# Optimization experiments

Hardware: AMD Instinct MI355X
Metric: run time of the kernel (lower is better)

The kernel has to match this reference:

```python
import jax, jax.numpy as jnp
import numpy as np

B_SZ, L, D_MODEL, D_STATE = 8, 2048, 1024, 64
LN_EPS = 1e-5


def setup_inputs() -> dict:
    key = jax.random.key(0)
    ks = jax.random.split(key, 12)
    x = jax.random.normal(ks[0], (B_SZ, L, D_MODEL), dtype=jnp.float32)
    # input projection (nn.Linear)
    W_in = jax.random.normal(ks[1], (D_MODEL, D_MODEL), dtype=jnp.float32) / np.sqrt(D_MODEL)
    b_in = jnp.zeros((D_MODEL,), dtype=jnp.float32)
    # LayerNorm affine
    gamma = jnp.ones((D_MODEL,), dtype=jnp.float32)
    beta = jnp.zeros((D_MODEL,), dtype=jnp.float32)
    # SSM params as real/imag pairs (torch stores cfloat); init per _init_state_space
    A_re = -jax.random.uniform(ks[2], (D_STATE,), dtype=jnp.float32) * 0.1
    A_im = jax.random.normal(ks[3], (D_STATE,), dtype=jnp.float32) * 0.1
    B_re = jax.random.normal(ks[4], (D_STATE,), dtype=jnp.float32) * 0.0004
    B_im = jax.random.normal(ks[5], (D_STATE,), dtype=jnp.float32) * 0.0004
    C_re = jax.random.normal(ks[6], (D_MODEL, D_STATE), dtype=jnp.float32) * 0.0004
    C_im = jax.random.normal(ks[7], (D_MODEL, D_STATE), dtype=jnp.float32) * 0.0004
    D_re = jax.random.normal(ks[8], (D_MODEL,), dtype=jnp.float32) * 0.02
    D_im = jax.random.normal(ks[9], (D_MODEL,), dtype=jnp.float32) * 0.02
    return {"x": x, "W_in": W_in, "b_in": b_in, "gamma": gamma, "beta": beta,
            "A_re": A_re, "A_im": A_im, "B_re": B_re, "B_im": B_im,
            "C_re": C_re, "C_im": C_im, "D_re": D_re, "D_im": D_im}


def _forward(x, W_in, b_in, gamma, beta, A_re, A_im, B_re, B_im, C_re, C_im, D_re, D_im):
    # input projection + LayerNorm
    x = jnp.einsum('bld,de->ble', x, W_in.T) + b_in
    mu = jnp.mean(x, axis=-1, keepdims=True)
    var = jnp.mean(jnp.square(x - mu), axis=-1, keepdims=True)
    x = (x - mu) * jax.lax.rsqrt(var + LN_EPS) * gamma + beta

    Lc = x.shape[1]
    A = A_re + 1j * A_im          # (N,)
    Bp = B_re + 1j * B_im         # (N,)
    Cp = C_re + 1j * C_im         # (M, N)
    Dp = D_re + 1j * D_im         # (M,)
    # A^l via exp(l * log A) -> (L, N), stable for autodiff
    pows = jnp.exp(jnp.arange(Lc, dtype=jnp.float32)[:, None] * jnp.log(A)[None, :])
    # fused kernel generation: K[l, m] = sum_n A^l[n] * B[n] * C[m, n]  (+ D broadcast on all taps, per source)
    K = jnp.einsum('ln,n,mn->lm', pows, Bp, Cp) + Dp[None, :]  # (L, M) complex

    # causal depthwise long convolution via FFT: y[t, m] = sum_{s<=t} K[s, m] * x[t-s, m]
    n = 2 * Lc
    Xf = jnp.fft.fft(x.astype(jnp.complex64), n=n, axis=1)   # (B, 2L, M)
    Kf = jnp.fft.fft(K, n=n, axis=0)                          # (2L, M)
    y = jnp.fft.ifft(Xf * Kf[None], axis=1)[:, :Lc, :].real   # real part (standard S4 convention)

    return y.astype(x.dtype) + x  # dropout=0 (eval); residual


def reference(x, W_in, b_in, gamma, beta, A_re, A_im, B_re, B_im, C_re, C_im, D_re, D_im):
    return _forward(x, W_in, b_in, gamma, beta, A_re, A_im, B_re, B_im, C_re, C_im, D_re, D_im)
```

## Files before the change

kernel.cpp:

```cpp
#include <hip/hip_runtime.h>
#include <stdint.h>


typedef __attribute__((ext_vector_type(8))) short short8;
typedef __attribute__((ext_vector_type(8))) unsigned short ushort8;
typedef __attribute__((ext_vector_type(4))) float f32x4;
typedef unsigned short ushort;

#define L_SEQ 2048
#define DM    1024
#define TT    8
#define NC    16
#define CL    128

__device__ __forceinline__ ushort f2bf(float f) {
  uint32_t u = __builtin_bit_cast(uint32_t, f);
  u += 0x7FFFu + ((u >> 16) & 1u);
  return (ushort)(u >> 16);
}
__device__ __forceinline__ float bf2f(ushort u) {
  uint32_t w = ((uint32_t)u) << 16;
  return __builtin_bit_cast(float, w);
}
__device__ __forceinline__ void gload16(const void* g, void* lds_p) {
  __builtin_amdgcn_global_load_lds(
      (const __attribute__((address_space(1))) uint32_t*)g,
      (__attribute__((address_space(3))) uint32_t*)lds_p, 16, 0, 0);
}

__global__ __launch_bounds__(256) void cvt_and_kgen(
    const float* __restrict__ x, const float* __restrict__ W,
    ushort* __restrict__ Xbf, ushort* __restrict__ Wbf,
    const float* __restrict__ A_re, const float* __restrict__ A_im,
    const float* __restrict__ B_re, const float* __restrict__ B_im,
    const float* __restrict__ C_re, const float* __restrict__ C_im,
    float* __restrict__ Khat, int nx8, int nw8, int cvtBlocks) {
  int blk = blockIdx.x;
  int tid = threadIdx.x;
  if (blk < cvtBlocks) {
    int i = blk * 256 + tid;
    const float* src; ushort* dst; int idx;
    if (i < nx8) { src = x; dst = Xbf; idx = i; }
    else         { src = W; dst = Wbf; idx = i - nx8; if (idx >= nw8) return; }
    const f32x4* s = (const f32x4*)src + (size_t)idx * 2;
    f32x4 a = s[0], b = s[1];
    ushort8 o;
    #pragma unroll
    for (int e = 0; e < 4; ++e) { o[e] = f2bf(a[e]); o[4 + e] = f2bf(b[e]); }
    *(ushort8*)(dst + (size_t)idx * 8) = o;
    return;
  }
  int s = blk - cvtBlocks;
  __shared__ float Pr[64], Pi[64];
  if (tid < 64) {
    float ar = A_re[tid], ai = A_im[tid];
    float pr, pi;
    if (s == 0) { pr = 1.f; pi = 0.f; }
    else {
      float r2 = ar * ar + ai * ai;
      float rsf = expf(0.5f * (float)s * logf(r2));
      float ang = (float)s * atan2f(ai, ar);
      pr = rsf * cosf(ang); pi = rsf * sinf(ang);
    }
    float br = B_re[tid], bi = B_im[tid];
    Pr[tid] = pr * br - pi * bi;
    Pi[tid] = pr * bi + pi * br;
  }
  __syncthreads();
  for (int m = tid; m < DM; m += 256) {
    const float* cr = C_re + (size_t)m * 64;
    const float* ci = C_im + (size_t)m * 64;
    float acc = 0.f;
    #pragma unroll
    for (int n = 0; n < 64; ++n) acc += Pr[n] * cr[n] - Pi[n] * ci[n];
    Khat[(size_t)s * DM + m] = acc;
  }
}

#define SBAR() do { asm volatile("" ::: "memory"); __builtin_amdgcn_s_barrier(); asm volatile("" ::: "memory"); } while (0)
#define LGKM0() asm volatile("s_waitcnt lgkmcnt(0)" ::: "memory")

#define RD_A(ABASE, MH)                                                            \
  { _Pragma("unroll") for (int mi_ = 0; mi_ < 4; ++mi_) {                          \
      int row_ = wr * 128 + (MH) * 64 + mi_ * 16 + fr;                             \
      const char* rp_ = (const char*)(ABASE) + row_ * 128;                         \
      _Pragma("unroll") for (int kk_ = 0; kk_ < 2; ++kk_) {                        \
        int slot_ = kk_ * 4 + kg;                                                  \
        areg[mi_][kk_] = *(const short8*)(rp_ + (((slot_ ^ (row_ & 7)) << 4)));    \
      } } }

#define RD_B(DST, BBASE, NH)                                                       \
  { _Pragma("unroll") for (int ni_ = 0; ni_ < 2; ++ni_) {                          \
      int row_ = wn * 64 + (NH) * 32 + ni_ * 16 + fr;                              \
      const char* rp_ = (const char*)(BBASE) + row_ * 128;                         \
      _Pragma("unroll") for (int kk_ = 0; kk_ < 2; ++kk_) {                        \
        int slot_ = kk_ * 4 + kg;                                                  \
        DST[ni_][kk_] = *(const short8*)(rp_ + (((slot_ ^ (row_ & 7)) << 4)));     \
      } } }

#define MF(MH, NH, BV)                                                             \
  { _Pragma("unroll") for (int mi_ = 0; mi_ < 4; ++mi_)                            \
      _Pragma("unroll") for (int ni_ = 0; ni_ < 2; ++ni_) {                        \
        acc[(MH)*4+mi_][(NH)*2+ni_] = __builtin_amdgcn_mfma_f32_16x16x32_bf16(     \
            areg[mi_][0], BV[ni_][0], acc[(MH)*4+mi_][(NH)*2+ni_], 0, 0, 0);       \
        acc[(MH)*4+mi_][(NH)*2+ni_] = __builtin_amdgcn_mfma_f32_16x16x32_bf16(     \
            areg[mi_][1], BV[ni_][1], acc[(MH)*4+mi_][(NH)*2+ni_], 0, 0, 0); } }

#define STAGE(LDSHALF, GROW, TTI)                                                  \
  { const ushort* g_ = (GROW) + (size_t)(wid * 16 + rl) * DM + (TTI) * 64 + sl * 8;\
    gload16(g_,          (LDSHALF) + wid * 1024);                                  \
    gload16(g_ + 8 * DM, (LDSHALF) + wid * 1024 + 512); }

__global__ __launch_bounds__(512, 2) void gemm_bias(const ushort* __restrict__ Xb,
                                                    const ushort* __restrict__ Wb,
                                                    const float* __restrict__ bias,
                                                    ushort* __restrict__ Yb,
                                                    float2* __restrict__ rowpart) {
  extern __shared__ ushort lds[];
  ushort* A0 = lds;
  ushort* B0 = lds + 16384;
  ushort* A1 = lds + 32768;
  ushort* B1 = lds + 49152;

  int wg = blockIdx.x;
  int swz = (wg & 7) * 32 + (wg >> 3);
  int bm = swz >> 2, bn = swz & 3;
  int tid = threadIdx.x;
  int lane = tid & 63, wid = tid >> 6;
  int wr = wid >> 2, wn = wid & 3;
  int fr = lane & 15, kg = lane >> 4;
  int rl = lane >> 3, sl = (lane & 7) ^ rl;

  const ushort* XgT = Xb + (size_t)(bm * 256) * DM;
  const ushort* XgB = XgT + (size_t)128 * DM;
  const ushort* WgT = Wb + (size_t)(bn * 256) * DM;
  const ushort* WgX = WgT + (size_t)128 * DM;

  f32x4 acc[8][4];
  #pragma unroll
  for (int i = 0; i < 8; ++i)
    #pragma unroll
    for (int j = 0; j < 4; ++j) acc[i][j] = (f32x4){0.f, 0.f, 0.f, 0.f};
  short8 areg[4][2], bt[2][2], bb[2][2];

  STAGE(A0,         XgT, 0);
  STAGE(A0 + 8192,  XgB, 0);
  STAGE(B0,         WgT, 0);
  STAGE(B0 + 8192,  WgX, 0);
  STAGE(B1,         WgT, 1);
  STAGE(B1 + 8192,  WgX, 1);
  asm volatile("s_waitcnt vmcnt(4)" ::: "memory");
  SBAR();

  #pragma unroll 1
  for (int t = 0; t < 8; ++t) {
    int o = 2 * t + 1, n0 = 2 * t + 2, n1 = 2 * t + 3;
    bool stg = (t < 7);
    RD_A(A0, 0); RD_B(bt, B0, 0);
    STAGE(A1, XgT, o);
    SBAR(); LGKM0();
    __builtin_amdgcn_s_setprio(1); MF(0, 0, bt); __builtin_amdgcn_s_setprio(0);
    SBAR();
    RD_B(bb, B0, 1);
    STAGE(A1 + 8192, XgB, o);
    SBAR(); LGKM0();
    __builtin_amdgcn_s_setprio(1); MF(0, 1, bb); __builtin_amdgcn_s_setprio(0);
    SBAR();
    RD_A(A0, 1);
    if (stg) STAGE(B0, WgT, n0);
    SBAR(); LGKM0();
    __builtin_amdgcn_s_setprio(1); MF(1, 1, bb); __builtin_amdgcn_s_setprio(0);
    SBAR();
    if (stg) {
      STAGE(B0 + 8192, WgX, n0);
      asm volatile("s_waitcnt vmcnt(4)" ::: "memory");
    } else {
      asm volatile("s_waitcnt vmcnt(0)" ::: "memory");
    }
    SBAR(); LGKM0();
    __builtin_amdgcn_s_setprio(1); MF(1, 0, bt); __builtin_amdgcn_s_setprio(0);
    SBAR();
    RD_A(A1, 0); RD_B(bt, B1, 0);
    if (stg) STAGE(A0, XgT, n0);
    SBAR(); LGKM0();
    __builtin_amdgcn_s_setprio(1); MF(0, 0, bt); __builtin_amdgcn_s_setprio(0);
    SBAR();
    RD_B(bb, B1, 1);
    if (stg) STAGE(A0 + 8192, XgB, n0);
    SBAR(); LGKM0();
    __builtin_amdgcn_s_setprio(1); MF(0, 1, bb); __builtin_amdgcn_s_setprio(0);
    SBAR();
    RD_A(A1, 1);
    if (stg) STAGE(B1, WgT, n1);
    SBAR(); LGKM0();
    __builtin_amdgcn_s_setprio(1); MF(1, 1, bb); __builtin_amdgcn_s_setprio(0);
    SBAR();
    if (stg) {
      STAGE(B1 + 8192, WgX, n1);
      asm volatile("s_waitcnt vmcnt(4)" ::: "memory");
    } else {
      asm volatile("s_waitcnt vmcnt(0)" ::: "memory");
    }
    SBAR(); LGKM0();
    __builtin_amdgcn_s_setprio(1); MF(1, 0, bt); __builtin_amdgcn_s_setprio(0);
    SBAR();
  }

  asm volatile("s_waitcnt vmcnt(0) lgkmcnt(0)" ::: "memory");
  __syncthreads();
  float* lsS = (float*)lds;
  float* lsQ = lsS + 1024;
  int fq = lane >> 4;
  float bv[4];
  #pragma unroll
  for (int ni = 0; ni < 4; ++ni) bv[ni] = bias[bn * 256 + wn * 64 + ni * 16 + fr];
  #pragma unroll
  for (int mi = 0; mi < 8; ++mi) {
    float rs_[4] = {0.f, 0.f, 0.f, 0.f}, rq_[4] = {0.f, 0.f, 0.f, 0.f};
    #pragma unroll
    for (int ni = 0; ni < 4; ++ni) {
      int gcol = bn * 256 + wn * 64 + ni * 16 + fr;
      #pragma unroll
      for (int j = 0; j < 4; ++j) {
        float v = acc[mi][ni][j] + bv[ni];
        int grow = bm * 256 + wr * 128 + mi * 16 + fq * 4 + j;
        Yb[(size_t)grow * DM + gcol] = f2bf(v);
        rs_[j] += v; rq_[j] += v * v;
      }
    }
    #pragma unroll
    for (int d = 1; d < 16; d <<= 1)
      #pragma unroll
      for (int j = 0; j < 4; ++j) {
        rs_[j] += __shfl_xor(rs_[j], d);
        rq_[j] += __shfl_xor(rq_[j], d);
      }
    if (fr == 0) {
      #pragma unroll
      for (int j = 0; j < 4; ++j) {
        int r = wr * 128 + mi * 16 + fq * 4 + j;
        lsS[wn * 256 + r] = rs_[j];
        lsQ[wn * 256 + r] = rq_[j];
      }
    }
  }
  __syncthreads();
  if (tid < 256) {
    float s = lsS[tid] + lsS[256 + tid] + lsS[512 + tid] + lsS[768 + tid];
    float q = lsQ[tid] + lsQ[256 + tid] + lsQ[512 + tid] + lsQ[768 + tid];
    rowpart[((size_t)(bm * 256 + tid)) * 4 + bn] = make_float2(s, q);
  }
}

__device__ __forceinline__ void row_stats(const float2* __restrict__ rowpart,
                                          int grow, float& mu_, float& rs_) {
  float s = 0.f, q = 0.f;
  #pragma unroll
  for (int n = 0; n < 4; ++n) { float2 p = rowpart[(size_t)grow * 4 + n]; s += p.x; q += p.y; }
  mu_ = s * (1.f / DM);
  float v = q * (1.f / DM) - mu_ * mu_;
  rs_ = rsqrtf(v + 1e-5f);
}

__global__ __launch_bounds__(256) void chunksum(const ushort* __restrict__ ybf,
                                                const float2* __restrict__ rowpart,
                                                const float* __restrict__ gamma,
                                                const float* __restrict__ beta,
                                                float* __restrict__ partial) {
  int blk = blockIdx.x;
  int b = blk >> 5, c = (blk >> 1) & 15, mg = blk & 1;
  int tid = threadIdx.x;
  int m2 = mg * 512 + tid * 2;
  int bb = b * L_SEQ, cs = c * CL;
  __shared__ float muL[CL], rsL[CL];
  if (tid < CL) row_stats(rowpart, bb + cs + tid, muL[tid], rsL[tid]);
  __syncthreads();
  float g0 = gamma[m2], g1 = gamma[m2 + 1], be0 = beta[m2], be1 = beta[m2 + 1];
  float s0 = 0.f, s1 = 0.f;
  const ushort* base = ybf + (size_t)(bb + cs) * DM + m2;
  #pragma unroll 8
  for (int t = 0; t < CL; ++t) {
    uint32_t v = *(const uint32_t*)(base + (size_t)t * DM);
    float f0 = bf2f((ushort)v), f1 = bf2f((ushort)(v >> 16));
    float r = rsL[t], mu_ = muL[t];
    s0 += (f0 - mu_) * r * g0 + be0;
    s1 += (f1 - mu_) * r * g1 + be1;
  }
  *(float2*)&partial[((size_t)(b * NC + c)) * DM + m2] = make_float2(s0, s1);
}

__global__ __launch_bounds__(256) void ssm2(const ushort* __restrict__ ybf,
                                            const float2* __restrict__ rowpart,
                                            const float* __restrict__ gamma,
                                            const float* __restrict__ beta,
                                            const float* __restrict__ Khat,
                                            const float* __restrict__ D_re,
                                            const float* __restrict__ partial,
                                            float* __restrict__ Out) {
  int blk = blockIdx.x;
  int b = blk >> 6, c = (blk >> 2) & 15, mg = blk & 3;
  int tid = threadIdx.x;
  int m = mg * 256 + tid;
  int bb = b * L_SEQ, cs = c * CL;

  __shared__ float muL[CL + TT], rsL[CL + TT];
  for (int r = tid; r < CL + TT; r += 256) {
    int row = cs - TT + r;
    if (row >= 0) row_stats(rowpart, bb + row, muL[r], rsL[r]);
    else { muL[r] = 0.f; rsL[r] = 0.f; }
  }
  __syncthreads();

  float kh[TT];
  #pragma unroll
  for (int s = 0; s < TT; ++s) kh[s] = Khat[(size_t)s * DM + m];
  float g = gamma[m], be = beta[m], dre = D_re[m];

  float run = 0.f;
  for (int cc = 0; cc < c; ++cc) run += partial[((size_t)(b * NC + cc)) * DM + m];

  float P[TT], A[32];
  if (c == 0) {
    #pragma unroll
    for (int i = 0; i < TT; ++i) P[i] = 0.f;
  } else {
    #pragma unroll
    for (int i = 0; i < TT; ++i) {
      float v = bf2f(ybf[(size_t)(bb + cs - TT + i) * DM + m]);
      P[i] = (v - muL[i]) * rsL[i] * g + be;
    }
  }
  #pragma unroll
  for (int i = 0; i < 32; ++i) {
    float v = bf2f(ybf[(size_t)(bb + cs + i) * DM + m]);
    A[i] = (v - muL[TT + i]) * rsL[TT + i] * g + be;
  }

  #pragma unroll 1
  for (int j = 0; j < CL / 32; ++j) {
    float B[32];
    if (j < CL / 32 - 1) {
      int tb = (j + 1) * 32;
      #pragma unroll
      for (int i = 0; i < 32; ++i) {
        float v = bf2f(ybf[(size_t)(bb + cs + tb + i) * DM + m]);
        B[i] = (v - muL[TT + tb + i]) * rsL[TT + tb + i] * g + be;
      }
    }
    #pragma unroll
    for (int i = 0; i < 32; ++i) {
      float fir = 0.f;
      #pragma unroll
      for (int s = 0; s < TT; ++s) {
        float xv = (i - s >= 0) ? A[i - s] : P[TT + i - s];
        fir += kh[s] * xv;
      }
      run += A[i];
      Out[(size_t)(bb + cs + j * 32 + i) * DM + m] = A[i] + fir + dre * run;
    }
    #pragma unroll
    for (int i = 0; i < TT; ++i) P[i] = A[32 - TT + i];
    #pragma unroll
    for (int i = 0; i < 32; ++i) A[i] = B[i];
  }
}

extern "C" void kernel_launch(void* const* d_in, const int* in_sizes, int n_in,
                              void* d_out, int out_size, void* d_ws, size_t ws_size,
                              hipStream_t stream) {
  const float* x     = (const float*)d_in[0];
  const float* W     = (const float*)d_in[1];
  const float* b_in  = (const float*)d_in[2];
  const float* gamma = (const float*)d_in[3];
  const float* beta  = (const float*)d_in[4];
  const float* A_re  = (const float*)d_in[5];
  const float* A_im  = (const float*)d_in[6];
  const float* B_re  = (const float*)d_in[7];
  const float* B_im  = (const float*)d_in[8];
  const float* C_re  = (const float*)d_in[9];
  const float* C_im  = (const float*)d_in[10];
  const float* D_re  = (const float*)d_in[11];

  char* ws = (char*)d_ws;
  float*  khat    = (float*)(ws + 0);
  ushort* Wbf     = (ushort*)(ws + 131072);
  ushort* ybf     = (ushort*)(ws + 2228224);
  float2* rowpart = (float2*)(ws + 35782656);
  float*  partial = (float*)(ws + 36306944);

  ushort* Xbf = (ushort*)d_out;
  float*  out = (float*)d_out;

  const int NX = 8 * L_SEQ * DM;
  const int NW = DM * DM;
  const int nx8 = NX / 8, nw8 = NW / 8;
  const int cvtBlocks = (nx8 + nw8) / 256;

  (void)hipFuncSetAttribute((const void*)gemm_bias,
                            hipFuncAttributeMaxDynamicSharedMemorySize, 131072);

  cvt_and_kgen<<<cvtBlocks + TT, 256, 0, stream>>>(x, W, Xbf, Wbf,
      A_re, A_im, B_re, B_im, C_re, C_im, khat, nx8, nw8, cvtBlocks);
  gemm_bias<<<256, 512, 131072, stream>>>(Xbf, Wbf, b_in, ybf, rowpart);
  chunksum<<<256, 256, 0, stream>>>(ybf, rowpart, gamma, beta, partial);
  ssm2<<<512, 256, 0, stream>>>(ybf, rowpart, gamma, beta, khat, D_re, partial, out);
}
```

Baseline: 110.8 us.

## Fuse kernel-tap generation into ssm2 and use multi-element fp32-to-bf16 conversion

Removes the separate K-tap generation blocks from the conversion kernel and recomputes the first TT taps inside each ssm2 block. A^s is now built by repeated complex multiplication instead of exp/log/atan2, and the Khat workspace buffer is dropped. The conversion kernel now processes four strided 32-byte chunks per thread, so it launches fewer blocks with more loads in flight. In exchange, every ssm2 block redoes a 64x8 dot-product per channel, reading C_re/C_im with a per-thread row stride that does not coalesce well.

After: 100.6 us. 9.3% less time.

```diff
diff --git a/kernel.cpp b/kernel.cpp
--- a/kernel.cpp
+++ b/kernel.cpp
@@ -28,52 +28,30 @@
       (__attribute__((address_space(3))) uint32_t*)lds_p, 16, 0, 0);
 }
 
-__global__ __launch_bounds__(256) void cvt_and_kgen(
-    const float* __restrict__ x, const float* __restrict__ W,
-    ushort* __restrict__ Xbf, ushort* __restrict__ Wbf,
-    const float* __restrict__ A_re, const float* __restrict__ A_im,
-    const float* __restrict__ B_re, const float* __restrict__ B_im,
-    const float* __restrict__ C_re, const float* __restrict__ C_im,
-    float* __restrict__ Khat, int nx8, int nw8, int cvtBlocks) {
+__global__ __launch_bounds__(256) void cvt_stream(const float* __restrict__ x,
+                                                  ushort* __restrict__ Xbf,
+                                                  const float* __restrict__ W,
+                                                  ushort* __restrict__ Wbf) {
   int blk = blockIdx.x;
-  int tid = threadIdx.x;
-  if (blk < cvtBlocks) {
-    int i = blk * 256 + tid;
-    const float* src; ushort* dst; int idx;
-    if (i < nx8) { src = x; dst = Xbf; idx = i; }
-    else         { src = W; dst = Wbf; idx = i - nx8; if (idx >= nw8) return; }
-    const f32x4* s = (const f32x4*)src + (size_t)idx * 2;
-    f32x4 a = s[0], b = s[1];
+  const float* src; ushort* dst; int bid, nb;
+  if (blk < 2048) { src = x; dst = Xbf; bid = blk; nb = 2048; }
+  else            { src = W; dst = Wbf; bid = blk - 2048; nb = 128; }
+  size_t base = (size_t)bid * 256 + threadIdx.x;
+  size_t stride = (size_t)nb * 256;
+  f32x4 a[4], b[4];
+  #pragma unroll
+  for (int it = 0; it < 4; ++it) {
+    size_t i = base + (size_t)it * stride;
+    a[it] = ((const f32x4*)src)[2 * i];
+    b[it] = ((const f32x4*)src)[2 * i + 1];
+  }
+  #pragma unroll
+  for (int it = 0; it < 4; ++it) {
+    size_t i = base + (size_t)it * stride;
     ushort8 o;
     #pragma unroll
-    for (int e = 0; e < 4; ++e) { o[e] = f2bf(a[e]); o[4 + e] = f2bf(b[e]); }
-    *(ushort8*)(dst + (size_t)idx * 8) = o;
-    return;
-  }
-  int s = blk - cvtBlocks;
-  __shared__ float Pr[64], Pi[64];
-  if (tid < 64) {
-    float ar = A_re[tid], ai = A_im[tid];
-    float pr, pi;
-    if (s == 0) { pr = 1.f; pi = 0.f; }
-    else {
-      float r2 = ar * ar + ai * ai;
-      float rsf = expf(0.5f * (float)s * logf(r2));
-      float ang = (float)s * atan2f(ai, ar);
-      pr = rsf * cosf(ang); pi = rsf * sinf(ang);
-    }
-    float br = B_re[tid], bi = B_im[tid];
-    Pr[tid] = pr * br - pi * bi;
-    Pi[tid] = pr * bi + pi * br;
-  }
-  __syncthreads();
-  for (int m = tid; m < DM; m += 256) {
-    const float* cr = C_re + (size_t)m * 64;
-    const float* ci = C_im + (size_t)m * 64;
-    float acc = 0.f;
-    #pragma unroll
-    for (int n = 0; n < 64; ++n) acc += Pr[n] * cr[n] - Pi[n] * ci[n];
-    Khat[(size_t)s * DM + m] = acc;
+    for (int e = 0; e < 4; ++e) { o[e] = f2bf(a[it][e]); o[4 + e] = f2bf(b[it][e]); }
+    ((ushort8*)dst)[i] = o;
   }
 }
 
@@ -293,7 +271,12 @@
                                             const float2* __restrict__ rowpart,
                                             const float* __restrict__ gamma,
                                             const float* __restrict__ beta,
-                                            const float* __restrict__ Khat,
+                                            const float* __restrict__ A_re,
+                                            const float* __restrict__ A_im,
+                                            const float* __restrict__ B_re,
+                                            const float* __restrict__ B_im,
+                                            const float* __restrict__ C_re,
+                                            const float* __restrict__ C_im,
                                             const float* __restrict__ D_re,
                                             const float* __restrict__ partial,
                                             float* __restrict__ Out) {
@@ -304,6 +287,20 @@
   int bb = b * L_SEQ, cs = c * CL;
 
   __shared__ float muL[CL + TT], rsL[CL + TT];
+  __shared__ float PrT[TT][64], PiT[TT][64];
+  if (tid < 64) {
+    float ar = A_re[tid], ai = A_im[tid];
+    float br = B_re[tid], bi = B_im[tid];
+    float pr = 1.f, pi = 0.f;
+    #pragma unroll
+    for (int s = 0; s < TT; ++s) {
+      PrT[s][tid] = pr * br - pi * bi;
+      PiT[s][tid] = pr * bi + pi * br;
+      float npr = pr * ar - pi * ai;
+      pi = pr * ai + pi * ar;
+      pr = npr;
+    }
+  }
   for (int r = tid; r < CL + TT; r += 256) {
     int row = cs - TT + r;
     if (row >= 0) row_stats(rowpart, bb + row, muL[r], rsL[r]);
@@ -313,7 +310,17 @@
 
   float kh[TT];
   #pragma unroll
-  for (int s = 0; s < TT; ++s) kh[s] = Khat[(size_t)s * DM + m];
+  for (int s = 0; s < TT; ++s) kh[s] = 0.f;
+  {
+    const float* cr = C_re + (size_t)m * 64;
+    const float* ci = C_im + (size_t)m * 64;
+    for (int n = 0; n < 64; ++n) {
+      float crv = cr[n], civ = ci[n];
+      #pragma unroll
+      for (int s = 0; s < TT; ++s) kh[s] += PrT[s][n] * crv - PiT[s][n] * civ;
+    }
+  }
+
   float g = gamma[m], be = beta[m], dre = D_re[m];
 
   float run = 0.f;
@@ -382,26 +389,21 @@
   const float* D_re  = (const float*)d_in[11];
 
   char* ws = (char*)d_ws;
-  float*  khat    = (float*)(ws + 0);
-  ushort* Wbf     = (ushort*)(ws + 131072);
-  ushort* ybf     = (ushort*)(ws + 2228224);
-  float2* rowpart = (float2*)(ws + 35782656);
-  float*  partial = (float*)(ws + 36306944);
+  ushort* Wbf     = (ushort*)(ws + 0);
+  ushort* ybf     = (ushort*)(ws + 2097152);
+  float2* rowpart = (float2*)(ws + 35651584);
+  float*  partial = (float*)(ws + 36175872);
 
   ushort* Xbf = (ushort*)d_out;
   float*  out = (float*)d_out;
 
-  const int NX = 8 * L_SEQ * DM;
-  const int NW = DM * DM;
-  const int nx8 = NX / 8, nw8 = NW / 8;
-  const int cvtBlocks = (nx8 + nw8) / 256;
-
   (void)hipFuncSetAttribute((const void*)gemm_bias,
                             hipFuncAttributeMaxDynamicSharedMemorySize, 131072);
 
-  cvt_and_kgen<<<cvtBlocks + TT, 256, 0, stream>>>(x, W, Xbf, Wbf,
-      A_re, A_im, B_re, B_im, C_re, C_im, khat, nx8, nw8, cvtBlocks);
+  cvt_stream<<<2176, 256, 0, stream>>>(x, Xbf, W, Wbf);
   gemm_bias<<<256, 512, 131072, stream>>>(Xbf, Wbf, b_in, ybf, rowpart);
   chunksum<<<256, 256, 0, stream>>>(ybf, rowpart, gamma, beta, partial);
-  ssm2<<<512, 256, 0, stream>>>(ybf, rowpart, gamma, beta, khat, D_re, partial, out);
-}
+  ssm2<<<512, 256, 0, stream>>>(ybf, rowpart, gamma, beta,
+                                A_re, A_im, B_re, B_im, C_re, C_im, D_re,
+                                partial, out);
+}
```

## Fuse fp32-to-bf16 conversion of activations into GEMM A-tile loading

Applied to the files above, without the earlier changes.

The separate pre-pass that converted all of x to bf16 is removed. The GEMM now loads fp32 x tiles into registers, converts them with packed bf16 conversion instructions, and writes them to swizzled LDS, so the extra read and write of the full activation tensor goes away. The cost is more GEMM register pressure and fp32 global loads that are twice as wide per tile, with LDS writes folded into the pipelined loop. The A^s power computation also changes from exp/log/atan2 to repeated complex multiplication.

Result: no change. 109.9 us (-0.9%).

```diff
diff --git a/kernel.cpp b/kernel.cpp
--- a/kernel.cpp
+++ b/kernel.cpp
@@ -28,40 +28,30 @@
       (__attribute__((address_space(3))) uint32_t*)lds_p, 16, 0, 0);
 }
 
-__global__ __launch_bounds__(256) void cvt_and_kgen(
-    const float* __restrict__ x, const float* __restrict__ W,
-    ushort* __restrict__ Xbf, ushort* __restrict__ Wbf,
+__global__ __launch_bounds__(256) void wcvt_kgen(
+    const float* __restrict__ W, ushort* __restrict__ Wbf,
     const float* __restrict__ A_re, const float* __restrict__ A_im,
     const float* __restrict__ B_re, const float* __restrict__ B_im,
     const float* __restrict__ C_re, const float* __restrict__ C_im,
-    float* __restrict__ Khat, int nx8, int nw8, int cvtBlocks) {
+    float* __restrict__ Khat) {
   int blk = blockIdx.x;
   int tid = threadIdx.x;
-  if (blk < cvtBlocks) {
+  if (blk < 512) {
     int i = blk * 256 + tid;
-    const float* src; ushort* dst; int idx;
-    if (i < nx8) { src = x; dst = Xbf; idx = i; }
-    else         { src = W; dst = Wbf; idx = i - nx8; if (idx >= nw8) return; }
-    const f32x4* s = (const f32x4*)src + (size_t)idx * 2;
+    const f32x4* s = (const f32x4*)W + (size_t)i * 2;
     f32x4 a = s[0], b = s[1];
     ushort8 o;
     #pragma unroll
     for (int e = 0; e < 4; ++e) { o[e] = f2bf(a[e]); o[4 + e] = f2bf(b[e]); }
-    *(ushort8*)(dst + (size_t)idx * 8) = o;
+    *(ushort8*)(Wbf + (size_t)i * 8) = o;
     return;
   }
-  int s = blk - cvtBlocks;
+  int s = blk - 512;
   __shared__ float Pr[64], Pi[64];
   if (tid < 64) {
     float ar = A_re[tid], ai = A_im[tid];
-    float pr, pi;
-    if (s == 0) { pr = 1.f; pi = 0.f; }
-    else {
-      float r2 = ar * ar + ai * ai;
-      float rsf = expf(0.5f * (float)s * logf(r2));
-      float ang = (float)s * atan2f(ai, ar);
-      pr = rsf * cosf(ang); pi = rsf * sinf(ang);
-    }
+    float pr = 1.f, pi = 0.f;
+    for (int k = 0; k < s; ++k) { float n = pr * ar - pi * ai; pi = pr * ai + pi * ar; pr = n; }
     float br = B_re[tid], bi = B_im[tid];
     Pr[tid] = pr * br - pi * bi;
     Pi[tid] = pr * bi + pi * br;
@@ -79,6 +69,7 @@
 
 #define SBAR() do { asm volatile("" ::: "memory"); __builtin_amdgcn_s_barrier(); asm volatile("" ::: "memory"); } while (0)
 #define LGKM0() asm volatile("s_waitcnt lgkmcnt(0)" ::: "memory")
+#define CVTPK(D, S0, S1) asm("v_cvt_pk_bf16_f32 %0, %1, %2" : "=v"(D) : "v"(S0), "v"(S1))
 
 #define RD_A(ABASE, MH)                                                            \
   { _Pragma("unroll") for (int mi_ = 0; mi_ < 4; ++mi_) {                          \
@@ -111,7 +102,28 @@
     gload16(g_,          (LDSHALF) + wid * 1024);                                  \
     gload16(g_ + 8 * DM, (LDSHALF) + wid * 1024 + 512); }
 
-__global__ __launch_bounds__(512, 2) void gemm_bias(const ushort* __restrict__ Xb,
+#define A_LOAD(TTI)                                                                \
+  { const float* gx_ = X + (size_t)(bm * 256 + wid * 16 + rl) * DM + (TTI) * 64 + ac8; \
+    av[0] = *(const f32x4*)(gx_);                                                  \
+    av[1] = *(const f32x4*)(gx_ + 4);                                              \
+    av[2] = *(const f32x4*)(gx_ + 8 * DM);                                         \
+    av[3] = *(const f32x4*)(gx_ + 8 * DM + 4);                                     \
+    av[4] = *(const f32x4*)(gx_ + 128 * DM);                                       \
+    av[5] = *(const f32x4*)(gx_ + 128 * DM + 4);                                   \
+    av[6] = *(const f32x4*)(gx_ + 136 * DM);                                       \
+    av[7] = *(const f32x4*)(gx_ + 136 * DM + 4); }
+
+#define A_WRITE(ABASE)                                                             \
+  { _Pragma("unroll") for (int rs_ = 0; rs_ < 4; ++rs_) {                          \
+      uint32_t p0_, p1_, p2_, p3_;                                                 \
+      f32x4 lo_ = av[2 * rs_], hi_ = av[2 * rs_ + 1];                              \
+      CVTPK(p0_, lo_[0], lo_[1]); CVTPK(p1_, lo_[2], lo_[3]);                      \
+      CVTPK(p2_, hi_[0], hi_[1]); CVTPK(p3_, hi_[2], hi_[3]);                      \
+      int boff_ = ((rs_ & 2) ? 16384 : 0)                                          \
+                + (wid * 16 + rl + ((rs_ & 1) ? 8 : 0)) * 128 + (lane & 7) * 16;   \
+      *(uint4*)((char*)(ABASE) + boff_) = make_uint4(p0_, p1_, p2_, p3_); } }
+
+__global__ __launch_bounds__(512, 2) void gemm_bias(const float* __restrict__ X,
                                                     const ushort* __restrict__ Wb,
                                                     const float* __restrict__ bias,
                                                     ushort* __restrict__ Yb,
@@ -130,9 +142,8 @@
   int wr = wid >> 2, wn = wid & 3;
   int fr = lane & 15, kg = lane >> 4;
   int rl = lane >> 3, sl = (lane & 7) ^ rl;
-
-  const ushort* XgT = Xb + (size_t)(bm * 256) * DM;
-  const ushort* XgB = XgT + (size_t)128 * DM;
+  int ac8 = ((lane & 7) ^ rl) * 8;
+
   const ushort* WgT = Wb + (size_t)(bn * 256) * DM;
   const ushort* WgX = WgT + (size_t)128 * DM;
 
@@ -142,14 +153,16 @@
     #pragma unroll
     for (int j = 0; j < 4; ++j) acc[i][j] = (f32x4){0.f, 0.f, 0.f, 0.f};
   short8 areg[4][2], bt[2][2], bb[2][2];
-
-  STAGE(A0,         XgT, 0);
-  STAGE(A0 + 8192,  XgB, 0);
+  f32x4 av[8];
+
+  A_LOAD(0);
   STAGE(B0,         WgT, 0);
   STAGE(B0 + 8192,  WgX, 0);
   STAGE(B1,         WgT, 1);
   STAGE(B1 + 8192,  WgX, 1);
   asm volatile("s_waitcnt vmcnt(4)" ::: "memory");
+  A_WRITE(A0);
+  LGKM0();
   SBAR();
 
   #pragma unroll 1
@@ -157,12 +170,11 @@
     int o = 2 * t + 1, n0 = 2 * t + 2, n1 = 2 * t + 3;
     bool stg = (t < 7);
     RD_A(A0, 0); RD_B(bt, B0, 0);
-    STAGE(A1, XgT, o);
+    A_LOAD(o);
     SBAR(); LGKM0();
     __builtin_amdgcn_s_setprio(1); MF(0, 0, bt); __builtin_amdgcn_s_setprio(0);
     SBAR();
     RD_B(bb, B0, 1);
-    STAGE(A1 + 8192, XgB, o);
     SBAR(); LGKM0();
     __builtin_amdgcn_s_setprio(1); MF(0, 1, bb); __builtin_amdgcn_s_setprio(0);
     SBAR();
@@ -177,16 +189,16 @@
     } else {
       asm volatile("s_waitcnt vmcnt(0)" ::: "memory");
     }
+    A_WRITE(A1);
     SBAR(); LGKM0();
     __builtin_amdgcn_s_setprio(1); MF(1, 0, bt); __builtin_amdgcn_s_setprio(0);
     SBAR();
     RD_A(A1, 0); RD_B(bt, B1, 0);
-    if (stg) STAGE(A0, XgT, n0);
+    if (stg) A_LOAD(n0);
     SBAR(); LGKM0();
     __builtin_amdgcn_s_setprio(1); MF(0, 0, bt); __builtin_amdgcn_s_setprio(0);
     SBAR();
     RD_B(bb, B1, 1);
-    if (stg) STAGE(A0 + 8192, XgB, n0);
     SBAR(); LGKM0();
     __builtin_amdgcn_s_setprio(1); MF(0, 1, bb); __builtin_amdgcn_s_setprio(0);
     SBAR();
@@ -198,6 +210,7 @@
     if (stg) {
       STAGE(B1 + 8192, WgX, n1);
       asm volatile("s_waitcnt vmcnt(4)" ::: "memory");
+      A_WRITE(A0);
     } else {
       asm volatile("s_waitcnt vmcnt(0)" ::: "memory");
     }
@@ -382,26 +395,20 @@
   const float* D_re  = (const float*)d_in[11];
 
   char* ws = (char*)d_ws;
-  float*  khat    = (float*)(ws + 0);
-  ushort* Wbf     = (ushort*)(ws + 131072);
-  ushort* ybf     = (ushort*)(ws + 2228224);
-  float2* rowpart = (float2*)(ws + 35782656);
-  float*  partial = (float*)(ws + 36306944);
-
-  ushort* Xbf = (ushort*)d_out;
-  float*  out = (float*)d_out;
-
-  const int NX = 8 * L_SEQ * DM;
-  const int NW = DM * DM;
-  const int nx8 = NX / 8, nw8 = NW / 8;
-  const int cvtBlocks = (nx8 + nw8) / 256;
+  ushort* Wbf     = (ushort*)(ws + 0);
+  ushort* ybf     = (ushort*)(ws + 2097152);
+  float2* rowpart = (float2*)(ws + 35651584);
+  float*  partial = (float*)(ws + 36175872);
+  float*  khat    = (float*)(ws + 36700160);
+
+  float* out = (float*)d_out;
 
   (void)hipFuncSetAttribute((const void*)gemm_bias,
                             hipFuncAttributeMaxDynamicSharedMemorySize, 131072);
 
-  cvt_and_kgen<<<cvtBlocks + TT, 256, 0, stream>>>(x, W, Xbf, Wbf,
-      A_re, A_im, B_re, B_im, C_re, C_im, khat, nx8, nw8, cvtBlocks);
-  gemm_bias<<<256, 512, 131072, stream>>>(Xbf, Wbf, b_in, ybf, rowpart);
+  wcvt_kgen<<<512 + TT, 256, 0, stream>>>(W, Wbf, A_re, A_im, B_re, B_im,
+                                          C_re, C_im, khat);
+  gemm_bias<<<256, 512, 131072, stream>>>(x, Wbf, b_in, ybf, rowpart);
   chunksum<<<256, 256, 0, stream>>>(ybf, rowpart, gamma, beta, partial);
   ssm2<<<512, 256, 0, stream>>>(ybf, rowpart, gamma, beta, khat, D_re, partial, out);
 }
```
